# Kernel tuning notes

Hardware: AMD Instinct MI355X
Metric: run time of the kernel (lower is better)

## Reference

```python
import jax, jax.numpy as jnp
import numpy as np

D_MODEL = 1024
NUM_HEADS = 16
HEAD_DIM = D_MODEL // NUM_HEADS
B, S = 2, 2048


def setup_inputs() -> dict:
    key = jax.random.key(0)
    ks = jax.random.split(key, 7)
    scale = 1.0 / np.sqrt(D_MODEL)
    return {
        "query": jax.random.normal(ks[0], (B, S, D_MODEL), jnp.float32),
        "key": jax.random.normal(ks[1], (B, S, D_MODEL), jnp.float32),
        "value": jax.random.normal(ks[2], (B, S, D_MODEL), jnp.float32),
        "Wq": jax.random.normal(ks[3], (D_MODEL, D_MODEL), jnp.float32) * scale,
        "Wk": jax.random.normal(ks[4], (D_MODEL, D_MODEL), jnp.float32) * scale,
        "Wv": jax.random.normal(ks[5], (D_MODEL, D_MODEL), jnp.float32) * scale,
        "Wo": jax.random.normal(ks[6], (D_MODEL, D_MODEL), jnp.float32) * scale,
    }


def reference(query, key, value, Wq, Wk, Wv, Wo):
    b, tl, _ = query.shape
    sl = key.shape[1]
    # Linear (no bias): x @ W.T, then split heads -> (B, H, L, Dh)
    def split_heads(x, L):
        return x.reshape(b, L, NUM_HEADS, HEAD_DIM).transpose(0, 2, 1, 3)
    Q = split_heads(query @ Wq.T, tl)
    K = split_heads(key @ Wk.T, sl)
    V = split_heads(value @ Wv.T, sl)
    scores = jnp.einsum("bhqd,bhkd->bhqk", Q, K) / jnp.sqrt(jnp.float32(HEAD_DIM))
    attn_weights = jax.nn.softmax(scores, axis=-1)
    # dropout is identity in eval mode
    context = jnp.einsum("bhqk,bhkd->bhqd", attn_weights, V)
    context = context.transpose(0, 2, 1, 3).reshape(b, tl, D_MODEL)
    output = context @ Wo.T
    return (output, attn_weights)
```

## Files before the change

kernel.cpp:

```cpp
#include <hip/hip_runtime.h>
#include <stdint.h>
#include <stddef.h>

#define D_MODEL 1024
#define NHEADS  16
#define HDIM    64
#define BB      2
#define SSEQ    2048

using bf16x8 = __attribute__((ext_vector_type(8))) short;
using f32x4  = __attribute__((ext_vector_type(4))) float;
using s16x4  = __attribute__((ext_vector_type(4))) short;

static __device__ __forceinline__ float b2f(short s) {
  union { float f; unsigned u; } v;
  v.u = ((unsigned)(unsigned short)s) << 16;
  return v.f;
}
static __device__ __forceinline__ short f2b(float f) {
  union { float f; unsigned u; } v;
  v.f = f;
  unsigned r = v.u + 0x7fffu + ((v.u >> 16) & 1u);
  return (short)(r >> 16);
}
static __device__ __forceinline__ unsigned rnd2(float a, float b, float* fa,
                                                float* fb) {
  union { float f; unsigned u; } x, y;
  x.f = a; y.f = b;
  const unsigned ra = (x.u + 0x7fffu + ((x.u >> 16) & 1u)) & 0xffff0000u;
  const unsigned rb = (y.u + 0x7fffu + ((y.u >> 16) & 1u)) & 0xffff0000u;
  x.u = ra; y.u = rb;
  *fa = x.f; *fb = y.f;
  return (ra >> 16) | rb;
}
static __device__ __forceinline__ float unlo(unsigned u) {
  union { float f; unsigned v; } x; x.v = u << 16; return x.f;
}
static __device__ __forceinline__ float unhi(unsigned u) {
  union { float f; unsigned v; } x; x.v = u & 0xffff0000u; return x.f;
}

static __device__ __forceinline__ void gload16(const void* g, void* l) {
  __builtin_amdgcn_global_load_lds(
      (const __attribute__((address_space(1))) unsigned int*)g,
      (__attribute__((address_space(3))) unsigned int*)l, 16, 0, 0);
}

__global__ __launch_bounds__(256) void k_cvt(const float* __restrict__ src,
                                             short* __restrict__ dst, int n4) {
  int i = blockIdx.x * blockDim.x + threadIdx.x;
  const int stride = gridDim.x * blockDim.x;
  for (; i < n4; i += stride) {
    const float4 v = ((const float4*)src)[i];
    s16x4 o;
    o[0] = f2b(v.x); o[1] = f2b(v.y); o[2] = f2b(v.z); o[3] = f2b(v.w);
    ((s16x4*)dst)[i] = o;
  }
}

template <bool F32OUT>
static __device__ __forceinline__ void gemm_bt_dev(
    const short* __restrict__ A, const short* __restrict__ W, void* __restrict__ Cv,
    int N, int K) {
  __shared__ short sA[128 * 32];
  __shared__ short sB[128 * 32];

  const int t  = threadIdx.x;
  const int l  = t & 63;
  const int w  = t >> 6;
  const int wm = w >> 1, wn = w & 1;
  const int g  = l >> 4, lr = l & 15;
  const int m0 = blockIdx.y * 128;
  const int n0 = blockIdx.x * 128;

  f32x4 acc[4][4];
#pragma unroll
  for (int i = 0; i < 4; ++i)
#pragma unroll
    for (int j = 0; j < 4; ++j) {
      acc[i][j][0] = 0.f; acc[i][j][1] = 0.f;
      acc[i][j][2] = 0.f; acc[i][j][3] = 0.f;
    }

  const int r0 = t >> 2;
  const int c0 = (t & 3) * 8;
  const short* ga0 = A + (size_t)(m0 + r0) * K + c0;
  const short* ga1 = A + (size_t)(m0 + 64 + r0) * K + c0;
  const short* gb0 = W + (size_t)(n0 + r0) * K + c0;
  const short* gb1 = W + (size_t)(n0 + 64 + r0) * K + c0;
  short* la0 = &sA[(t & ~63) * 8];
  short* la1 = la0 + 256 * 8;
  short* lb0 = &sB[(t & ~63) * 8];
  short* lb1 = lb0 + 256 * 8;

  for (int k0 = 0; k0 < K; k0 += 32) {
    __syncthreads();
    gload16(ga0 + k0, la0);
    gload16(ga1 + k0, la1);
    gload16(gb0 + k0, lb0);
    gload16(gb1 + k0, lb1);
    __syncthreads();

    bf16x8 af[4], bfr[4];
#pragma unroll
    for (int i = 0; i < 4; ++i)
      af[i] = *(const bf16x8*)&sA[(wm * 64 + i * 16 + lr) * 32 + g * 8];
#pragma unroll
    for (int i = 0; i < 4; ++i)
      bfr[i] = *(const bf16x8*)&sB[(wn * 64 + i * 16 + lr) * 32 + g * 8];
#pragma unroll
    for (int i = 0; i < 4; ++i)
#pragma unroll
      for (int j = 0; j < 4; ++j)
        acc[i][j] = __builtin_amdgcn_mfma_f32_16x16x32_bf16(af[i], bfr[j],
                                                            acc[i][j], 0, 0, 0);
  }

#pragma unroll
  for (int i = 0; i < 4; ++i)
#pragma unroll
    for (int j = 0; j < 4; ++j)
#pragma unroll
      for (int rr = 0; rr < 4; ++rr) {
        const int row = m0 + wm * 64 + i * 16 + g * 4 + rr;
        const int col = n0 + wn * 64 + j * 16 + lr;
        if (F32OUT)
          ((float*)Cv)[(size_t)row * N + col] = acc[i][j][rr];
        else
          ((short*)Cv)[(size_t)row * N + col] = f2b(acc[i][j][rr]);
      }
}

__global__ __launch_bounds__(256) void k_gemm_f32out(
    const short* __restrict__ A, const short* __restrict__ W,
    float* __restrict__ C, int N, int K) {
  gemm_bt_dev<true>(A, W, C, N, K);
}

__global__ __launch_bounds__(256) void k_gemm_qkv(
    const short* __restrict__ q, const short* __restrict__ k,
    const short* __restrict__ v, const short* __restrict__ wq,
    const short* __restrict__ wk, const short* __restrict__ wv,
    short* __restrict__ Qb, short* __restrict__ Kb, short* __restrict__ Vb) {
  const short *A, *W;
  short* C;
  if (blockIdx.z == 0)      { A = q; W = wq; C = Qb; }
  else if (blockIdx.z == 1) { A = k; W = wk; C = Kb; }
  else                      { A = v; W = wv; C = Vb; }
  gemm_bt_dev<false>(A, W, C, D_MODEL, D_MODEL);
}

__global__ __launch_bounds__(256) void k_transpose_v(
    const short* __restrict__ Vb, short* __restrict__ Vt) {
  __shared__ short tile[64][66];
  const int bh = blockIdx.x;
  const int b = bh >> 4, h = bh & 15;
  const int s0 = blockIdx.y * 64;
  const int t = threadIdx.x;
#pragma unroll
  for (int i = 0; i < 16; ++i) {
    int e = t + i * 256;
    int si = e >> 6, dj = e & 63;
    tile[si][dj] = Vb[((size_t)b * SSEQ + s0 + si) * D_MODEL + h * HDIM + dj];
  }
  __syncthreads();
#pragma unroll
  for (int i = 0; i < 16; ++i) {
    int e = t + i * 256;
    int dj = e >> 6, si = e & 63;
    Vt[((size_t)bh * HDIM + dj) * SSEQ + s0 + si] = tile[si][dj];
  }
}

__global__ __launch_bounds__(256) void k_attn(
    const short* __restrict__ Qb, const short* __restrict__ Kb,
    const short* __restrict__ Vt, float* __restrict__ attnO,
    short* __restrict__ ctx) {
  __shared__ __attribute__((aligned(16))) short ptile[4][16][40];
  __shared__ float wmx[4][16];
  __shared__ float wls[4][16];
  __shared__ f32x4 red[4][4][64];

  const int t = threadIdx.x;
  const int l = t & 63, w = t >> 6;
  const int g = l >> 4, lr = l & 15;
  const int orig = blockIdx.x;
  const int id = (orig & 7) * 512 + (orig >> 3);
  const int q0 = (id & 127) * 16;
  const int bh = id >> 7;
  const int b = bh >> 4, h = bh & 15;

  const size_t qoff = ((size_t)b * SSEQ + q0 + lr) * D_MODEL + h * HDIM;
  const bf16x8 aq0 = *(const bf16x8*)&Qb[qoff + g * 8];
  const bf16x8 aq1 = *(const bf16x8*)&Qb[qoff + 32 + g * 8];

  const short* Kh = Kb + (size_t)b * SSEQ * D_MODEL + h * HDIM;
  const short* Vh = Vt + (size_t)bh * HDIM * SSEQ;
  const int kbase = w * 512;

  unsigned sreg[64];
  float pm = -1e30f, pl = 0.f;
#pragma unroll
  for (int st = 0; st < 16; ++st) {
    const int n0 = kbase + st * 32;
    const short* kr0 = Kh + (size_t)(n0 + lr) * D_MODEL;
    const short* kr1 = Kh + (size_t)(n0 + 16 + lr) * D_MODEL;
    const bf16x8 ka0 = *(const bf16x8*)&kr0[g * 8];
    const bf16x8 ka1 = *(const bf16x8*)&kr0[32 + g * 8];
    const bf16x8 kb0 = *(const bf16x8*)&kr1[g * 8];
    const bf16x8 kb1 = *(const bf16x8*)&kr1[32 + g * 8];
    f32x4 sA, sB;
    sA[0] = 0.f; sA[1] = 0.f; sA[2] = 0.f; sA[3] = 0.f;
    sB[0] = 0.f; sB[1] = 0.f; sB[2] = 0.f; sB[3] = 0.f;
    sA = __builtin_amdgcn_mfma_f32_16x16x32_bf16(ka0, aq0, sA, 0, 0, 0);
    sA = __builtin_amdgcn_mfma_f32_16x16x32_bf16(ka1, aq1, sA, 0, 0, 0);
    sB = __builtin_amdgcn_mfma_f32_16x16x32_bf16(kb0, aq0, sB, 0, 0, 0);
    sB = __builtin_amdgcn_mfma_f32_16x16x32_bf16(kb1, aq1, sB, 0, 0, 0);
    float v0, v1, v2, v3, v4, v5, v6, v7;
    sreg[st * 4 + 0] = rnd2(sA[0] * 0.125f, sA[1] * 0.125f, &v0, &v1);
    sreg[st * 4 + 1] = rnd2(sA[2] * 0.125f, sA[3] * 0.125f, &v2, &v3);
    sreg[st * 4 + 2] = rnd2(sB[0] * 0.125f, sB[1] * 0.125f, &v4, &v5);
    sreg[st * 4 + 3] = rnd2(sB[2] * 0.125f, sB[3] * 0.125f, &v6, &v7);
    const float mx = fmaxf(fmaxf(fmaxf(v0, v1), fmaxf(v2, v3)),
                           fmaxf(fmaxf(v4, v5), fmaxf(v6, v7)));
    const float nm = fmaxf(pm, mx);
    const float s = __expf(v0 - nm) + __expf(v1 - nm) + __expf(v2 - nm) +
                    __expf(v3 - nm) + __expf(v4 - nm) + __expf(v5 - nm) +
                    __expf(v6 - nm) + __expf(v7 - nm);
    pl = pl * __expf(pm - nm) + s;
    pm = nm;
  }
#pragma unroll
  for (int mask = 16; mask <= 32; mask <<= 1) {
    const float om = __shfl_xor(pm, mask, 64);
    const float ol = __shfl_xor(pl, mask, 64);
    const float nm = fmaxf(pm, om);
    pl = pl * __expf(pm - nm) + ol * __expf(om - nm);
    pm = nm;
  }
  if (l < 16) { wmx[w][lr] = pm; wls[w][lr] = pl; }
  __syncthreads();

  float M, inv;
  {
    const float m0 = wmx[0][lr], m1 = wmx[1][lr];
    const float m2 = wmx[2][lr], m3 = wmx[3][lr];
    M = fmaxf(fmaxf(m0, m1), fmaxf(m2, m3));
    const float L = wls[0][lr] * __expf(m0 - M) + wls[1][lr] * __expf(m1 - M) +
                    wls[2][lr] * __expf(m2 - M) + wls[3][lr] * __expf(m3 - M);
    inv = 1.f / L;
  }

  f32x4 accO[4];
#pragma unroll
  for (int u = 0; u < 4; ++u) {
    accO[u][0] = 0.f; accO[u][1] = 0.f; accO[u][2] = 0.f; accO[u][3] = 0.f;
  }
  float* arow = attnO + ((size_t)bh * SSEQ + q0 + lr) * SSEQ;

#pragma unroll
  for (int st = 0; st < 16; ++st) {
    const int n0 = kbase + st * 32;
    const bf16x8 bv0 = *(const bf16x8*)&Vh[(size_t)(lr) * SSEQ + n0 + g * 8];
    const bf16x8 bv1 = *(const bf16x8*)&Vh[(size_t)(16 + lr) * SSEQ + n0 + g * 8];
    const bf16x8 bv2 = *(const bf16x8*)&Vh[(size_t)(32 + lr) * SSEQ + n0 + g * 8];
    const bf16x8 bv3 = *(const bf16x8*)&Vh[(size_t)(48 + lr) * SSEQ + n0 + g * 8];

    const unsigned u0 = sreg[st * 4 + 0], u1 = sreg[st * 4 + 1];
    const unsigned u2 = sreg[st * 4 + 2], u3 = sreg[st * 4 + 3];
    const float pa0 = __expf(unlo(u0) - M) * inv;
    const float pa1 = __expf(unhi(u0) - M) * inv;
    const float pa2 = __expf(unlo(u1) - M) * inv;
    const float pa3 = __expf(unhi(u1) - M) * inv;
    const float pa4 = __expf(unlo(u2) - M) * inv;
    const float pa5 = __expf(unhi(u2) - M) * inv;
    const float pa6 = __expf(unlo(u3) - M) * inv;
    const float pa7 = __expf(unhi(u3) - M) * inv;

    float4 s0, s1;
    s0.x = pa0; s0.y = pa1; s0.z = pa2; s0.w = pa3;
    s1.x = pa4; s1.y = pa5; s1.z = pa6; s1.w = pa7;
    *(float4*)(arow + n0 + g * 4) = s0;
    *(float4*)(arow + n0 + 16 + g * 4) = s1;

    s16x4 h0, h1;
    h0[0] = f2b(pa0); h0[1] = f2b(pa1); h0[2] = f2b(pa2); h0[3] = f2b(pa3);
    h1[0] = f2b(pa4); h1[1] = f2b(pa5); h1[2] = f2b(pa6); h1[3] = f2b(pa7);
    *(s16x4*)&ptile[w][lr][g * 4] = h0;
    *(s16x4*)&ptile[w][lr][16 + g * 4] = h1;
    const bf16x8 ap = *(const bf16x8*)&ptile[w][lr][g * 8];
    accO[0] = __builtin_amdgcn_mfma_f32_16x16x32_bf16(ap, bv0, accO[0], 0, 0, 0);
    accO[1] = __builtin_amdgcn_mfma_f32_16x16x32_bf16(ap, bv1, accO[1], 0, 0, 0);
    accO[2] = __builtin_amdgcn_mfma_f32_16x16x32_bf16(ap, bv2, accO[2], 0, 0, 0);
    accO[3] = __builtin_amdgcn_mfma_f32_16x16x32_bf16(ap, bv3, accO[3], 0, 0, 0);
  }

#pragma unroll
  for (int u = 0; u < 4; ++u) red[w][u][l] = accO[u];
  __syncthreads();
  {
    f32x4 o = red[0][w][l];
    const f32x4 o1 = red[1][w][l], o2 = red[2][w][l], o3 = red[3][w][l];
    o[0] += o1[0] + o2[0] + o3[0];
    o[1] += o1[1] + o2[1] + o3[1];
    o[2] += o1[2] + o2[2] + o3[2];
    o[3] += o1[3] + o2[3] + o3[3];
#pragma unroll
    for (int rr = 0; rr < 4; ++rr) {
      const int qr = q0 + g * 4 + rr;
      ctx[((size_t)b * SSEQ + qr) * D_MODEL + h * HDIM + w * 16 + lr] =
          f2b(o[rr]);
    }
  }
}

extern "C" void kernel_launch(void* const* d_in, const int* in_sizes, int n_in,
                              void* d_out, int out_size, void* d_ws,
                              size_t ws_size, hipStream_t stream) {
  const float* qf  = (const float*)d_in[0];
  const float* kf  = (const float*)d_in[1];
  const float* vf  = (const float*)d_in[2];
  const float* wqf = (const float*)d_in[3];
  const float* wkf = (const float*)d_in[4];
  const float* wvf = (const float*)d_in[5];
  const float* wof = (const float*)d_in[6];

  float* out  = (float*)d_out;
  float* attn = out + (size_t)BB * SSEQ * D_MODEL;

  const size_t NTOK = (size_t)BB * SSEQ;
  const size_t XN = NTOK * D_MODEL;
  const size_t WN = (size_t)D_MODEL * D_MODEL;

  short* qb  = (short*)d_ws;
  short* kb  = qb + XN;
  short* vb  = kb + XN;
  short* wqb = vb + XN;
  short* wkb = wqb + WN;
  short* wvb = wkb + WN;
  short* wob = wvb + WN;
  short* Qb  = wob + WN;
  short* Kb  = Qb + XN;
  short* Vb  = Kb + XN;
  short* Vt  = Vb + XN;
  short* ctx = Vt + XN;

  k_cvt<<<512, 256, 0, stream>>>(qf, qb, (int)(XN / 4));
  k_cvt<<<512, 256, 0, stream>>>(kf, kb, (int)(XN / 4));
  k_cvt<<<512, 256, 0, stream>>>(vf, vb, (int)(XN / 4));
  k_cvt<<<256, 256, 0, stream>>>(wqf, wqb, (int)(WN / 4));
  k_cvt<<<256, 256, 0, stream>>>(wkf, wkb, (int)(WN / 4));
  k_cvt<<<256, 256, 0, stream>>>(wvf, wvb, (int)(WN / 4));
  k_cvt<<<256, 256, 0, stream>>>(wof, wob, (int)(WN / 4));

  k_gemm_qkv<<<dim3(D_MODEL / 128, NTOK / 128, 3), 256, 0, stream>>>(
      qb, kb, vb, wqb, wkb, wvb, Qb, Kb, Vb);
  k_transpose_v<<<dim3(BB * NHEADS, SSEQ / 64), 256, 0, stream>>>(Vb, Vt);
  k_attn<<<4096, 256, 0, stream>>>(Qb, Kb, Vt, attn, ctx);
  k_gemm_f32out<<<dim3(D_MODEL / 128, NTOK / 128), 256, 0, stream>>>(
      ctx, wob, out, D_MODEL, D_MODEL);
}
```

Baseline: 886.8 us.

## Split attention into stats pass and emit pass recomputing QK scores

Splits the single attention kernel into two kernels. The first computes the row max and then the row sum of exponentials and stores per-row M and 1/L. The second recomputes the QK^T scores with MFMA, then writes probabilities and accumulates P·V. This removes the 64-register score buffer from the emit kernel and the online-softmax rescaling, which should lower register pressure and raise occupancy. The cost is that the QK^T matmul and K loads run twice, plus an extra launch and a small round trip through global memory. The per-row stats reuse the qb workspace buffer, which is dead once the projection GEMM has finished.

```diff
diff --git a/kernel.cpp b/kernel.cpp
--- a/kernel.cpp
+++ b/kernel.cpp
@@ -172,15 +172,11 @@
   }
 }
 
-__global__ __launch_bounds__(256) void k_attn(
+__global__ __launch_bounds__(256) void k_attn_stats(
     const short* __restrict__ Qb, const short* __restrict__ Kb,
-    const short* __restrict__ Vt, float* __restrict__ attnO,
-    short* __restrict__ ctx) {
-  __shared__ __attribute__((aligned(16))) short ptile[4][16][40];
+    float* __restrict__ Mrow, float* __restrict__ Irow) {
   __shared__ float wmx[4][16];
   __shared__ float wls[4][16];
-  __shared__ f32x4 red[4][4][64];
-
   const int t = threadIdx.x;
   const int l = t & 63, w = t >> 6;
   const int g = l >> 4, lr = l & 15;
@@ -193,13 +189,11 @@
   const size_t qoff = ((size_t)b * SSEQ + q0 + lr) * D_MODEL + h * HDIM;
   const bf16x8 aq0 = *(const bf16x8*)&Qb[qoff + g * 8];
   const bf16x8 aq1 = *(const bf16x8*)&Qb[qoff + 32 + g * 8];
-
   const short* Kh = Kb + (size_t)b * SSEQ * D_MODEL + h * HDIM;
-  const short* Vh = Vt + (size_t)bh * HDIM * SSEQ;
   const int kbase = w * 512;
 
   unsigned sreg[64];
-  float pm = -1e30f, pl = 0.f;
+  float pm = -1e30f;
 #pragma unroll
   for (int st = 0; st < 16; ++st) {
     const int n0 = kbase + st * 32;
@@ -221,35 +215,64 @@
     sreg[st * 4 + 1] = rnd2(sA[2] * 0.125f, sA[3] * 0.125f, &v2, &v3);
     sreg[st * 4 + 2] = rnd2(sB[0] * 0.125f, sB[1] * 0.125f, &v4, &v5);
     sreg[st * 4 + 3] = rnd2(sB[2] * 0.125f, sB[3] * 0.125f, &v6, &v7);
-    const float mx = fmaxf(fmaxf(fmaxf(v0, v1), fmaxf(v2, v3)),
-                           fmaxf(fmaxf(v4, v5), fmaxf(v6, v7)));
-    const float nm = fmaxf(pm, mx);
-    const float s = __expf(v0 - nm) + __expf(v1 - nm) + __expf(v2 - nm) +
-                    __expf(v3 - nm) + __expf(v4 - nm) + __expf(v5 - nm) +
-                    __expf(v6 - nm) + __expf(v7 - nm);
-    pl = pl * __expf(pm - nm) + s;
-    pm = nm;
-  }
-#pragma unroll
-  for (int mask = 16; mask <= 32; mask <<= 1) {
-    const float om = __shfl_xor(pm, mask, 64);
-    const float ol = __shfl_xor(pl, mask, 64);
-    const float nm = fmaxf(pm, om);
-    pl = pl * __expf(pm - nm) + ol * __expf(om - nm);
-    pm = nm;
-  }
-  if (l < 16) { wmx[w][lr] = pm; wls[w][lr] = pl; }
+    pm = fmaxf(pm, fmaxf(fmaxf(fmaxf(v0, v1), fmaxf(v2, v3)),
+                         fmaxf(fmaxf(v4, v5), fmaxf(v6, v7))));
+  }
+#pragma unroll
+  for (int mask = 16; mask <= 32; mask <<= 1)
+    pm = fmaxf(pm, __shfl_xor(pm, mask, 64));
+  if (l < 16) wmx[w][lr] = pm;
   __syncthreads();
-
-  float M, inv;
-  {
-    const float m0 = wmx[0][lr], m1 = wmx[1][lr];
-    const float m2 = wmx[2][lr], m3 = wmx[3][lr];
-    M = fmaxf(fmaxf(m0, m1), fmaxf(m2, m3));
-    const float L = wls[0][lr] * __expf(m0 - M) + wls[1][lr] * __expf(m1 - M) +
-                    wls[2][lr] * __expf(m2 - M) + wls[3][lr] * __expf(m3 - M);
-    inv = 1.f / L;
-  }
+  const float M = fmaxf(fmaxf(wmx[0][lr], wmx[1][lr]),
+                        fmaxf(wmx[2][lr], wmx[3][lr]));
+
+  float s0 = 0.f, s1 = 0.f, s2 = 0.f, s3 = 0.f;
+#pragma unroll
+  for (int st = 0; st < 16; ++st) {
+    const unsigned u0 = sreg[st * 4 + 0], u1 = sreg[st * 4 + 1];
+    const unsigned u2 = sreg[st * 4 + 2], u3 = sreg[st * 4 + 3];
+    s0 += __expf(unlo(u0) - M) + __expf(unhi(u0) - M);
+    s1 += __expf(unlo(u1) - M) + __expf(unhi(u1) - M);
+    s2 += __expf(unlo(u2) - M) + __expf(unhi(u2) - M);
+    s3 += __expf(unlo(u3) - M) + __expf(unhi(u3) - M);
+  }
+  float sum = (s0 + s1) + (s2 + s3);
+#pragma unroll
+  for (int mask = 16; mask <= 32; mask <<= 1) sum += __shfl_xor(sum, mask, 64);
+  if (l < 16) wls[w][lr] = sum;
+  __syncthreads();
+  if (w == 0 && l < 16) {
+    const float L = (wls[0][lr] + wls[1][lr]) + (wls[2][lr] + wls[3][lr]);
+    Mrow[(size_t)bh * SSEQ + q0 + lr] = M;
+    Irow[(size_t)bh * SSEQ + q0 + lr] = 1.f / L;
+  }
+}
+
+__global__ __launch_bounds__(256) void k_attn_emit(
+    const short* __restrict__ Qb, const short* __restrict__ Kb,
+    const short* __restrict__ Vt, const float* __restrict__ Mrow,
+    const float* __restrict__ Irow, float* __restrict__ attnO,
+    short* __restrict__ ctx) {
+  __shared__ __attribute__((aligned(16))) short ptile[4][16][40];
+  __shared__ f32x4 red[4][4][64];
+  const int t = threadIdx.x;
+  const int l = t & 63, w = t >> 6;
+  const int g = l >> 4, lr = l & 15;
+  const int orig = blockIdx.x;
+  const int id = (orig & 7) * 512 + (orig >> 3);
+  const int q0 = (id & 127) * 16;
+  const int bh = id >> 7;
+  const int b = bh >> 4, h = bh & 15;
+
+  const size_t qoff = ((size_t)b * SSEQ + q0 + lr) * D_MODEL + h * HDIM;
+  const bf16x8 aq0 = *(const bf16x8*)&Qb[qoff + g * 8];
+  const bf16x8 aq1 = *(const bf16x8*)&Qb[qoff + 32 + g * 8];
+  const short* Kh = Kb + (size_t)b * SSEQ * D_MODEL + h * HDIM;
+  const short* Vh = Vt + (size_t)bh * HDIM * SSEQ;
+  const int kbase = w * 512;
+
+  const float M = Mrow[(size_t)bh * SSEQ + q0 + lr];
+  const float inv = Irow[(size_t)bh * SSEQ + q0 + lr];
 
   f32x4 accO[4];
 #pragma unroll
@@ -261,27 +284,44 @@
 #pragma unroll
   for (int st = 0; st < 16; ++st) {
     const int n0 = kbase + st * 32;
+    const short* kr0 = Kh + (size_t)(n0 + lr) * D_MODEL;
+    const short* kr1 = Kh + (size_t)(n0 + 16 + lr) * D_MODEL;
+    const bf16x8 ka0 = *(const bf16x8*)&kr0[g * 8];
+    const bf16x8 ka1 = *(const bf16x8*)&kr0[32 + g * 8];
+    const bf16x8 kb0 = *(const bf16x8*)&kr1[g * 8];
+    const bf16x8 kb1 = *(const bf16x8*)&kr1[32 + g * 8];
     const bf16x8 bv0 = *(const bf16x8*)&Vh[(size_t)(lr) * SSEQ + n0 + g * 8];
     const bf16x8 bv1 = *(const bf16x8*)&Vh[(size_t)(16 + lr) * SSEQ + n0 + g * 8];
     const bf16x8 bv2 = *(const bf16x8*)&Vh[(size_t)(32 + lr) * SSEQ + n0 + g * 8];
     const bf16x8 bv3 = *(const bf16x8*)&Vh[(size_t)(48 + lr) * SSEQ + n0 + g * 8];
 
-    const unsigned u0 = sreg[st * 4 + 0], u1 = sreg[st * 4 + 1];
-    const unsigned u2 = sreg[st * 4 + 2], u3 = sreg[st * 4 + 3];
-    const float pa0 = __expf(unlo(u0) - M) * inv;
-    const float pa1 = __expf(unhi(u0) - M) * inv;
-    const float pa2 = __expf(unlo(u1) - M) * inv;
-    const float pa3 = __expf(unhi(u1) - M) * inv;
-    const float pa4 = __expf(unlo(u2) - M) * inv;
-    const float pa5 = __expf(unhi(u2) - M) * inv;
-    const float pa6 = __expf(unlo(u3) - M) * inv;
-    const float pa7 = __expf(unhi(u3) - M) * inv;
-
-    float4 s0, s1;
-    s0.x = pa0; s0.y = pa1; s0.z = pa2; s0.w = pa3;
-    s1.x = pa4; s1.y = pa5; s1.z = pa6; s1.w = pa7;
-    *(float4*)(arow + n0 + g * 4) = s0;
-    *(float4*)(arow + n0 + 16 + g * 4) = s1;
+    f32x4 sA, sB;
+    sA[0] = 0.f; sA[1] = 0.f; sA[2] = 0.f; sA[3] = 0.f;
+    sB[0] = 0.f; sB[1] = 0.f; sB[2] = 0.f; sB[3] = 0.f;
+    sA = __builtin_amdgcn_mfma_f32_16x16x32_bf16(ka0, aq0, sA, 0, 0, 0);
+    sA = __builtin_amdgcn_mfma_f32_16x16x32_bf16(ka1, aq1, sA, 0, 0, 0);
+    sB = __builtin_amdgcn_mfma_f32_16x16x32_bf16(kb0, aq0, sB, 0, 0, 0);
+    sB = __builtin_amdgcn_mfma_f32_16x16x32_bf16(kb1, aq1, sB, 0, 0, 0);
+
+    float v0, v1, v2, v3, v4, v5, v6, v7;
+    (void)rnd2(sA[0] * 0.125f, sA[1] * 0.125f, &v0, &v1);
+    (void)rnd2(sA[2] * 0.125f, sA[3] * 0.125f, &v2, &v3);
+    (void)rnd2(sB[0] * 0.125f, sB[1] * 0.125f, &v4, &v5);
+    (void)rnd2(sB[2] * 0.125f, sB[3] * 0.125f, &v6, &v7);
+    const float pa0 = __expf(v0 - M) * inv;
+    const float pa1 = __expf(v1 - M) * inv;
+    const float pa2 = __expf(v2 - M) * inv;
+    const float pa3 = __expf(v3 - M) * inv;
+    const float pa4 = __expf(v4 - M) * inv;
+    const float pa5 = __expf(v5 - M) * inv;
+    const float pa6 = __expf(v6 - M) * inv;
+    const float pa7 = __expf(v7 - M) * inv;
+
+    float4 w0, w1;
+    w0.x = pa0; w0.y = pa1; w0.z = pa2; w0.w = pa3;
+    w1.x = pa4; w1.y = pa5; w1.z = pa6; w1.w = pa7;
+    *(float4*)(arow + n0 + g * 4) = w0;
+    *(float4*)(arow + n0 + 16 + g * 4) = w1;
 
     s16x4 h0, h1;
     h0[0] = f2b(pa0); h0[1] = f2b(pa1); h0[2] = f2b(pa2); h0[3] = f2b(pa3);
@@ -344,6 +384,8 @@
   short* Vb  = Kb + XN;
   short* Vt  = Vb + XN;
   short* ctx = Vt + XN;
+  float* Mrow = (float*)qb;
+  float* Irow = Mrow + (size_t)BB * NHEADS * SSEQ;
 
   k_cvt<<<512, 256, 0, stream>>>(qf, qb, (int)(XN / 4));
   k_cvt<<<512, 256, 0, stream>>>(kf, kb, (int)(XN / 4));
@@ -356,7 +398,8 @@
   k_gemm_qkv<<<dim3(D_MODEL / 128, NTOK / 128, 3), 256, 0, stream>>>(
       qb, kb, vb, wqb, wkb, wvb, Qb, Kb, Vb);
   k_transpose_v<<<dim3(BB * NHEADS, SSEQ / 64), 256, 0, stream>>>(Vb, Vt);
-  k_attn<<<4096, 256, 0, stream>>>(Qb, Kb, Vt, attn, ctx);
+  k_attn_stats<<<4096, 256, 0, stream>>>(Qb, Kb, Mrow, Irow);
+  k_attn_emit<<<4096, 256, 0, stream>>>(Qb, Kb, Vt, Mrow, Irow, attn, ctx);
   k_gemm_f32out<<<dim3(D_MODEL / 128, NTOK / 128), 256, 0, stream>>>(
       ctx, wob, out, D_MODEL, D_MODEL);
 }
```

Measured after the change: 979.1 us. +10.4%, slower.
